# Performance work log

Measured on AMD Instinct MI355X. Metric: run time of the kernel, lower is better.

Reference implementation:

```python
import jax, jax.numpy as jnp
import numpy as np

BETA = 0.25
CODEBOOK_SIZE = 4096
EMBED_DIM = 32


def setup_inputs() -> dict:
    key = jax.random.key(0)
    k_z, k_t = jax.random.split(key)
    z = jax.random.normal(k_z, (16, EMBED_DIM, 64, 64), dtype=jnp.float32)
    table = jax.random.normal(k_t, (CODEBOOK_SIZE, EMBED_DIM), dtype=jnp.float32)
    return {"z": z, "table": table}


def reference(z, table):
    B, C, H, W = z.shape
    # [B,C,H,W] -> [B,H,W,C] -> [N,C]
    z_flat = jnp.transpose(z, (0, 2, 3, 1)).reshape(-1, C)
    # squared-distance: ||z||^2 + ||e||^2 - 2 z.e^T  -> [N, K]
    distances = (
        jnp.sum(z_flat * z_flat, axis=1, keepdims=True)
        + jnp.sum(table * table, axis=1)
        - 2.0 * jnp.einsum("nc,kc->nk", z_flat, table)
    )
    indices = jnp.argmin(distances, axis=1)          # [N]
    z_q_raw = table[indices]                         # [N, C]

    codebook_loss = jnp.mean((jax.lax.stop_gradient(z_flat) - z_q_raw) ** 2)
    commitment_loss = jnp.mean((z_flat - jax.lax.stop_gradient(z_q_raw)) ** 2)
    total_loss = codebook_loss + BETA * commitment_loss

    # straight-through estimator
    z_q = z_flat + jax.lax.stop_gradient(z_q_raw - z_flat)
    z_q = jnp.transpose(z_q.reshape(B, H, W, C), (0, 3, 1, 2))  # [B,C,H,W]
    per_back_indices = indices.reshape(B, -1)
    return z_q, per_back_indices, total_loss
```

## Files before the change

### kernel.cpp

```cpp
#include <hip/hip_runtime.h>
#include <hip/hip_bf16.h>

#define CDIM 32
#define KCODES 4096
#define NROWS 65536
#define HW 4096
#define KP 8
#define KSLICE (KCODES / KP)
#define TPB 256
#define RPT 2
#define ROWS_PER_BLOCK (TPB * RPT)
#define TILE 64
#define BETA 0.25f

#define LOSS_OFF  0u
#define BIAS_OFF  256u
#define SCORE_OFF (256u + KCODES * 4u)
#define IDX_OFF   (SCORE_OFF + (unsigned)KP * NROWS * 4u)
#define Z2_OFF    (IDX_OFF + (unsigned)KP * NROWS * 4u)

__global__ __launch_bounds__(256) void vq_bias(const float* __restrict__ table,
                                               float* __restrict__ bias) {
    int k = blockIdx.x * 256 + threadIdx.x;
    if (k >= KCODES) return;
    const float4* row = (const float4*)(table + (size_t)k * CDIM);
    float s = 0.f;
#pragma unroll
    for (int i = 0; i < CDIM / 4; ++i) {
        float4 v = row[i];
        s = fmaf(v.x, v.x, s);
        s = fmaf(v.y, v.y, s);
        s = fmaf(v.z, v.z, s);
        s = fmaf(v.w, v.w, s);
    }
    bias[k] = -0.5f * s;
}

__global__ __launch_bounds__(TPB) void vq_main(const float* __restrict__ z,
                                               const float* __restrict__ table,
                                               const float* __restrict__ bias,
                                               float* __restrict__ scores,
                                               int* __restrict__ idxs,
                                               float* __restrict__ z2out) {
    __shared__ float elds[TILE * CDIM];
    __shared__ float blds[TILE];

    const int t = threadIdx.x;
    const int rb = blockIdx.x * ROWS_PER_BLOCK;
    const int kp = blockIdx.y;
    const int k0 = kp * KSLICE;
    const int n0 = rb + t;
    const int n1 = n0 + TPB;
    const int b  = rb >> 12;
    const int hw0 = n0 & (HW - 1);
    const int hw1 = n1 & (HW - 1);
    const float* zb = z + (size_t)b * CDIM * HW;

    float z0[CDIM], z1[CDIM];
#pragma unroll
    for (int c = 0; c < CDIM; ++c) {
        z0[c] = zb[c * HW + hw0];
        z1[c] = zb[c * HW + hw1];
    }

    float best0 = -1e30f, best1 = -1e30f;
    int bi0 = 0, bi1 = 0;

    for (int kt = 0; kt < KSLICE; kt += TILE) {
        __syncthreads();
        const float4* src = (const float4*)(table + (size_t)(k0 + kt) * CDIM);
        float4* dst = (float4*)elds;
        dst[t] = src[t];
        dst[t + TPB] = src[t + TPB];
        if (t < TILE) blds[t] = bias[k0 + kt + t];
        __syncthreads();

#pragma unroll 2
        for (int kk = 0; kk < TILE; ++kk) {
            float a0 = blds[kk];
            float a1 = a0;
            const float* e = elds + kk * CDIM;
#pragma unroll
            for (int c = 0; c < CDIM; ++c) {
                float ev = e[c];
                a0 = fmaf(z0[c], ev, a0);
                a1 = fmaf(z1[c], ev, a1);
            }
            int k = k0 + kt + kk;
            if (a0 > best0) { best0 = a0; bi0 = k; }
            if (a1 > best1) { best1 = a1; bi1 = k; }
        }
    }

    scores[kp * NROWS + n0] = best0;
    scores[kp * NROWS + n1] = best1;
    idxs[kp * NROWS + n0] = bi0;
    idxs[kp * NROWS + n1] = bi1;

    if (kp == 0) {
        float s0 = 0.f, s1 = 0.f;
#pragma unroll
        for (int c = 0; c < CDIM; ++c) {
            s0 = fmaf(z0[c], z0[c], s0);
            s1 = fmaf(z1[c], z1[c], s1);
        }
        z2out[n0] = s0;
        z2out[n1] = s1;
    }
}

__global__ __launch_bounds__(256) void vq_combine(const float* __restrict__ scores,
                                                  const int* __restrict__ idxs,
                                                  const float* __restrict__ z2,
                                                  const float* __restrict__ table,
                                                  float* __restrict__ out_zq,
                                                  float* __restrict__ out_idx,
                                                  float* __restrict__ loss) {
    const int n = blockIdx.x * 256 + threadIdx.x;
    float best = -1e30f;
    int bi = 0;
#pragma unroll
    for (int kp = 0; kp < KP; ++kp) {
        float s = scores[kp * NROWS + n];
        int i = idxs[kp * NROWS + n];
        if (s > best) { best = s; bi = i; }
    }

    out_idx[n] = (float)bi;

    const int b = n >> 12;
    const int hw = n & (HW - 1);
    const float4* trow = (const float4*)(table + (size_t)bi * CDIM);
#pragma unroll
    for (int c4 = 0; c4 < CDIM / 4; ++c4) {
        float4 v = trow[c4];
        float* o = out_zq + ((size_t)(b * CDIM + c4 * 4) * HW + hw);
        o[0]        = v.x;
        o[HW]       = v.y;
        o[2 * HW]   = v.z;
        o[3 * HW]   = v.w;
    }

    float d = fmaxf(z2[n] - 2.0f * best, 0.0f);
#pragma unroll
    for (int off = 32; off; off >>= 1) d += __shfl_down(d, off);
    if ((threadIdx.x & 63) == 0) atomicAdd(loss, d);
}

__global__ void vq_finalize(const float* __restrict__ loss,
                            float* __restrict__ out_loss) {
    out_loss[0] = loss[0] * (1.0f + BETA) / (float)((size_t)NROWS * CDIM);
}

extern "C" void kernel_launch(void* const* d_in, const int* in_sizes, int n_in,
                              void* d_out, int out_size, void* d_ws, size_t ws_size,
                              hipStream_t stream) {
    const float* z     = (const float*)d_in[0];
    const float* table = (const float*)d_in[1];

    char* ws = (char*)d_ws;
    float* loss   = (float*)(ws + LOSS_OFF);
    float* bias   = (float*)(ws + BIAS_OFF);
    float* scores = (float*)(ws + SCORE_OFF);
    int*   idxs   = (int*)(ws + IDX_OFF);
    float* z2     = (float*)(ws + Z2_OFF);

    float* out_zq   = (float*)d_out;
    float* out_idx  = out_zq + (size_t)NROWS * CDIM;
    float* out_loss = out_idx + NROWS;

    hipMemsetAsync(loss, 0, sizeof(float), stream);

    vq_bias<<<KCODES / 256, 256, 0, stream>>>(table, bias);

    dim3 grid(NROWS / ROWS_PER_BLOCK, KP);
    vq_main<<<grid, TPB, 0, stream>>>(z, table, bias, scores, idxs, z2);

    vq_combine<<<NROWS / 256, 256, 0, stream>>>(scores, idxs, z2, table,
                                                out_zq, out_idx, loss);

    vq_finalize<<<1, 1, 0, stream>>>(loss, out_loss);
}
```

Measured before the change: 310.3 us.

## Use 2D register-tiled 4x4 outer-product distance kernel without K-split

Replaces the per-thread row scan (each thread holding two z rows, reading codebook entries from LDS) with a 64x64 tile scheme. Each thread computes a 4x4 block of rows by codes as outer products from transposed LDS tiles of z and the codebook. It then does a shuffle-based argmax across the 16 code-lanes with lowest-index tie-breaking. The K-split over 8 slices and its partial-score merge are removed, and the combine kernel now recomputes ||z||^2 from z itself. This raises FMA-to-LDS-load ratio but iterates all 4096 codes per block with a barrier per 64-code tile.

After: 324.0 us. 1.04x slower.

```diff
diff --git a/kernel.cpp b/kernel.cpp
--- a/kernel.cpp
+++ b/kernel.cpp
@@ -5,19 +5,15 @@
 #define KCODES 4096
 #define NROWS 65536
 #define HW 4096
-#define KP 8
-#define KSLICE (KCODES / KP)
 #define TPB 256
-#define RPT 2
-#define ROWS_PER_BLOCK (TPB * RPT)
-#define TILE 64
+#define RTILE 64
+#define KTILE 64
 #define BETA 0.25f
 
 #define LOSS_OFF  0u
 #define BIAS_OFF  256u
-#define SCORE_OFF (256u + KCODES * 4u)
-#define IDX_OFF   (SCORE_OFF + (unsigned)KP * NROWS * 4u)
-#define Z2_OFF    (IDX_OFF + (unsigned)KP * NROWS * 4u)
+#define SCORE_OFF (BIAS_OFF + KCODES * 4u)
+#define IDX_OFF   (SCORE_OFF + (unsigned)NROWS * 4u)
 
 __global__ __launch_bounds__(256) void vq_bias(const float* __restrict__ table,
                                                float* __restrict__ bias) {
@@ -36,112 +32,145 @@
     bias[k] = -0.5f * s;
 }
 
-__global__ __launch_bounds__(TPB) void vq_main(const float* __restrict__ z,
-                                               const float* __restrict__ table,
-                                               const float* __restrict__ bias,
-                                               float* __restrict__ scores,
-                                               int* __restrict__ idxs,
-                                               float* __restrict__ z2out) {
-    __shared__ float elds[TILE * CDIM];
-    __shared__ float blds[TILE];
-
-    const int t = threadIdx.x;
-    const int rb = blockIdx.x * ROWS_PER_BLOCK;
-    const int kp = blockIdx.y;
-    const int k0 = kp * KSLICE;
-    const int n0 = rb + t;
-    const int n1 = n0 + TPB;
-    const int b  = rb >> 12;
-    const int hw0 = n0 & (HW - 1);
-    const int hw1 = n1 & (HW - 1);
-    const float* zb = z + (size_t)b * CDIM * HW;
-
-    float z0[CDIM], z1[CDIM];
-#pragma unroll
-    for (int c = 0; c < CDIM; ++c) {
-        z0[c] = zb[c * HW + hw0];
-        z1[c] = zb[c * HW + hw1];
-    }
-
-    float best0 = -1e30f, best1 = -1e30f;
-    int bi0 = 0, bi1 = 0;
-
-    for (int kt = 0; kt < KSLICE; kt += TILE) {
+__global__ __launch_bounds__(TPB, 4) void vq_main(const float* __restrict__ z,
+                                                  const float* __restrict__ table,
+                                                  const float* __restrict__ bias,
+                                                  float* __restrict__ scores,
+                                                  int* __restrict__ idxs) {
+    __shared__ __align__(16) float zt[CDIM][RTILE];
+    __shared__ __align__(16) float et[CDIM][KTILE];
+    __shared__ __align__(16) float blds[KTILE];
+
+    const int t  = threadIdx.x;
+    const int tx = t & 15;
+    const int ty = t >> 4;
+    const int row0 = blockIdx.x * RTILE;
+    const int b   = row0 >> 12;
+    const int hw0 = row0 & (HW - 1);
+    const float* zb = z + (size_t)b * CDIM * HW + hw0;
+
+    {
+        int c = t >> 4, q = t & 15;
+        float4 v0 = *(const float4*)(zb + (size_t)c * HW + q * 4);
+        *(float4*)&zt[c][q * 4] = v0;
+        float4 v1 = *(const float4*)(zb + (size_t)(c + 16) * HW + q * 4);
+        *(float4*)&zt[c + 16][q * 4] = v1;
+    }
+
+    float best[4] = {-1e30f, -1e30f, -1e30f, -1e30f};
+    int   bi[4]   = {0, 0, 0, 0};
+
+    for (int k0 = 0; k0 < KCODES; k0 += KTILE) {
         __syncthreads();
-        const float4* src = (const float4*)(table + (size_t)(k0 + kt) * CDIM);
-        float4* dst = (float4*)elds;
-        dst[t] = src[t];
-        dst[t + TPB] = src[t + TPB];
-        if (t < TILE) blds[t] = bias[k0 + kt + t];
+        {
+            int k = t & 63, c4 = t >> 6;
+            const float* er = table + (size_t)(k0 + k) * CDIM;
+            float4 v = *(const float4*)(er + c4 * 4);
+            et[c4 * 4 + 0][k] = v.x;
+            et[c4 * 4 + 1][k] = v.y;
+            et[c4 * 4 + 2][k] = v.z;
+            et[c4 * 4 + 3][k] = v.w;
+            float4 w = *(const float4*)(er + (c4 + 4) * 4);
+            et[(c4 + 4) * 4 + 0][k] = w.x;
+            et[(c4 + 4) * 4 + 1][k] = w.y;
+            et[(c4 + 4) * 4 + 2][k] = w.z;
+            et[(c4 + 4) * 4 + 3][k] = w.w;
+            if (t < 16) *(float4*)&blds[t * 4] = *(const float4*)(bias + k0 + t * 4);
+        }
         __syncthreads();
 
-#pragma unroll 2
-        for (int kk = 0; kk < TILE; ++kk) {
-            float a0 = blds[kk];
-            float a1 = a0;
-            const float* e = elds + kk * CDIM;
-#pragma unroll
-            for (int c = 0; c < CDIM; ++c) {
-                float ev = e[c];
-                a0 = fmaf(z0[c], ev, a0);
-                a1 = fmaf(z1[c], ev, a1);
+        float4 bv = *(const float4*)&blds[tx * 4];
+        float acc[4][4];
+#pragma unroll
+        for (int j = 0; j < 4; ++j) {
+            acc[j][0] = bv.x; acc[j][1] = bv.y; acc[j][2] = bv.z; acc[j][3] = bv.w;
+        }
+
+#pragma unroll
+        for (int c = 0; c < CDIM; ++c) {
+            float4 zv = *(const float4*)&zt[c][ty * 4];
+            float4 ev = *(const float4*)&et[c][tx * 4];
+            acc[0][0] = fmaf(zv.x, ev.x, acc[0][0]);
+            acc[0][1] = fmaf(zv.x, ev.y, acc[0][1]);
+            acc[0][2] = fmaf(zv.x, ev.z, acc[0][2]);
+            acc[0][3] = fmaf(zv.x, ev.w, acc[0][3]);
+            acc[1][0] = fmaf(zv.y, ev.x, acc[1][0]);
+            acc[1][1] = fmaf(zv.y, ev.y, acc[1][1]);
+            acc[1][2] = fmaf(zv.y, ev.z, acc[1][2]);
+            acc[1][3] = fmaf(zv.y, ev.w, acc[1][3]);
+            acc[2][0] = fmaf(zv.z, ev.x, acc[2][0]);
+            acc[2][1] = fmaf(zv.z, ev.y, acc[2][1]);
+            acc[2][2] = fmaf(zv.z, ev.z, acc[2][2]);
+            acc[2][3] = fmaf(zv.z, ev.w, acc[2][3]);
+            acc[3][0] = fmaf(zv.w, ev.x, acc[3][0]);
+            acc[3][1] = fmaf(zv.w, ev.y, acc[3][1]);
+            acc[3][2] = fmaf(zv.w, ev.z, acc[3][2]);
+            acc[3][3] = fmaf(zv.w, ev.w, acc[3][3]);
+        }
+
+#pragma unroll
+        for (int j = 0; j < 4; ++j) {
+#pragma unroll
+            for (int i = 0; i < 4; ++i) {
+                int k = k0 + tx * 4 + i;
+                if (acc[j][i] > best[j]) { best[j] = acc[j][i]; bi[j] = k; }
             }
-            int k = k0 + kt + kk;
-            if (a0 > best0) { best0 = a0; bi0 = k; }
-            if (a1 > best1) { best1 = a1; bi1 = k; }
-        }
-    }
-
-    scores[kp * NROWS + n0] = best0;
-    scores[kp * NROWS + n1] = best1;
-    idxs[kp * NROWS + n0] = bi0;
-    idxs[kp * NROWS + n1] = bi1;
-
-    if (kp == 0) {
-        float s0 = 0.f, s1 = 0.f;
-#pragma unroll
-        for (int c = 0; c < CDIM; ++c) {
-            s0 = fmaf(z0[c], z0[c], s0);
-            s1 = fmaf(z1[c], z1[c], s1);
-        }
-        z2out[n0] = s0;
-        z2out[n1] = s1;
+        }
+    }
+
+#pragma unroll
+    for (int j = 0; j < 4; ++j) {
+        float s = best[j];
+        int   i = bi[j];
+#pragma unroll
+        for (int m = 1; m <= 8; m <<= 1) {
+            float s2 = __shfl_xor(s, m);
+            int   i2 = __shfl_xor(i, m);
+            if (s2 > s || (s2 == s && i2 < i)) { s = s2; i = i2; }
+        }
+        if (tx == 0) {
+            int n = row0 + ty * 4 + j;
+            scores[n] = s;
+            idxs[n]   = i;
+        }
     }
 }
 
 __global__ __launch_bounds__(256) void vq_combine(const float* __restrict__ scores,
                                                   const int* __restrict__ idxs,
-                                                  const float* __restrict__ z2,
+                                                  const float* __restrict__ z,
                                                   const float* __restrict__ table,
                                                   float* __restrict__ out_zq,
                                                   float* __restrict__ out_idx,
                                                   float* __restrict__ loss) {
     const int n = blockIdx.x * 256 + threadIdx.x;
-    float best = -1e30f;
-    int bi = 0;
-#pragma unroll
-    for (int kp = 0; kp < KP; ++kp) {
-        float s = scores[kp * NROWS + n];
-        int i = idxs[kp * NROWS + n];
-        if (s > best) { best = s; bi = i; }
-    }
-
-    out_idx[n] = (float)bi;
-
+    const int bi = idxs[n];
+    const float best = scores[n];
     const int b = n >> 12;
     const int hw = n & (HW - 1);
+
+    const float* zb = z + (size_t)b * CDIM * HW + hw;
+    float z2 = 0.f;
+#pragma unroll
+    for (int c = 0; c < CDIM; ++c) {
+        float v = zb[(size_t)c * HW];
+        z2 = fmaf(v, v, z2);
+    }
+
+    out_idx[n] = (float)bi;
+
     const float4* trow = (const float4*)(table + (size_t)bi * CDIM);
+    float* o = out_zq + (size_t)b * CDIM * HW + hw;
 #pragma unroll
     for (int c4 = 0; c4 < CDIM / 4; ++c4) {
         float4 v = trow[c4];
-        float* o = out_zq + ((size_t)(b * CDIM + c4 * 4) * HW + hw);
-        o[0]        = v.x;
-        o[HW]       = v.y;
-        o[2 * HW]   = v.z;
-        o[3 * HW]   = v.w;
-    }
-
-    float d = fmaxf(z2[n] - 2.0f * best, 0.0f);
+        o[(size_t)(c4 * 4 + 0) * HW] = v.x;
+        o[(size_t)(c4 * 4 + 1) * HW] = v.y;
+        o[(size_t)(c4 * 4 + 2) * HW] = v.z;
+        o[(size_t)(c4 * 4 + 3) * HW] = v.w;
+    }
+
+    float d = fmaxf(z2 - 2.0f * best, 0.0f);
 #pragma unroll
     for (int off = 32; off; off >>= 1) d += __shfl_down(d, off);
     if ((threadIdx.x & 63) == 0) atomicAdd(loss, d);
@@ -163,7 +192,6 @@
     float* bias   = (float*)(ws + BIAS_OFF);
     float* scores = (float*)(ws + SCORE_OFF);
     int*   idxs   = (int*)(ws + IDX_OFF);
-    float* z2     = (float*)(ws + Z2_OFF);
 
     float* out_zq   = (float*)d_out;
     float* out_idx  = out_zq + (size_t)NROWS * CDIM;
@@ -172,12 +200,8 @@
     hipMemsetAsync(loss, 0, sizeof(float), stream);
 
     vq_bias<<<KCODES / 256, 256, 0, stream>>>(table, bias);
-
-    dim3 grid(NROWS / ROWS_PER_BLOCK, KP);
-    vq_main<<<grid, TPB, 0, stream>>>(z, table, bias, scores, idxs, z2);
-
-    vq_combine<<<NROWS / 256, 256, 0, stream>>>(scores, idxs, z2, table,
+    vq_main<<<NROWS / RTILE, TPB, 0, stream>>>(z, table, bias, scores, idxs);
+    vq_combine<<<NROWS / 256, 256, 0, stream>>>(scores, idxs, z, table,
                                                 out_zq, out_idx, loss);
-
     vq_finalize<<<1, 1, 0, stream>>>(loss, out_loss);
 }
```

## Replace LDS codebook tiling with wave-uniform global loads and move z-norm to combine

Applied to the files above, without the earlier changes.

The main distance kernel no longer stages codebook tiles in shared memory with barriers. Each thread streams codebook rows directly from global memory at a wave-uniform index, so the compiler can use scalar loads and broadcast operands. Rows are paired as adjacent elements and loaded with float2, and the squared norm of z is computed in the combine kernel instead of a workspace buffer. This trades LDS traffic and synchronization for reliance on the scalar/L1 cache, and adds an extra read of z in combine.

Result: faster. 285.4 us (-8.0%).

```diff
diff --git a/kernel.cpp b/kernel.cpp
--- a/kernel.cpp
+++ b/kernel.cpp
@@ -8,16 +8,12 @@
 #define KP 8
 #define KSLICE (KCODES / KP)
 #define TPB 256
-#define RPT 2
-#define ROWS_PER_BLOCK (TPB * RPT)
-#define TILE 64
 #define BETA 0.25f
 
 #define LOSS_OFF  0u
 #define BIAS_OFF  256u
-#define SCORE_OFF (256u + KCODES * 4u)
+#define SCORE_OFF (BIAS_OFF + KCODES * 4u)
 #define IDX_OFF   (SCORE_OFF + (unsigned)KP * NROWS * 4u)
-#define Z2_OFF    (IDX_OFF + (unsigned)KP * NROWS * 4u)
 
 __global__ __launch_bounds__(256) void vq_bias(const float* __restrict__ table,
                                                float* __restrict__ bias) {
@@ -36,82 +32,54 @@
     bias[k] = -0.5f * s;
 }
 
-__global__ __launch_bounds__(TPB) void vq_main(const float* __restrict__ z,
-                                               const float* __restrict__ table,
-                                               const float* __restrict__ bias,
-                                               float* __restrict__ scores,
-                                               int* __restrict__ idxs,
-                                               float* __restrict__ z2out) {
-    __shared__ float elds[TILE * CDIM];
-    __shared__ float blds[TILE];
-
-    const int t = threadIdx.x;
-    const int rb = blockIdx.x * ROWS_PER_BLOCK;
-    const int kp = blockIdx.y;
-    const int k0 = kp * KSLICE;
-    const int n0 = rb + t;
-    const int n1 = n0 + TPB;
-    const int b  = rb >> 12;
-    const int hw0 = n0 & (HW - 1);
-    const int hw1 = n1 & (HW - 1);
-    const float* zb = z + (size_t)b * CDIM * HW;
+__global__ __launch_bounds__(TPB, 2) void vq_main(const float* __restrict__ z,
+                                                  const float* __restrict__ table,
+                                                  const float* __restrict__ bias,
+                                                  float* __restrict__ scores,
+                                                  int* __restrict__ idxs) {
+    const int t    = threadIdx.x;
+    const int kp   = blockIdx.y;
+    const int row0 = blockIdx.x * (TPB * 2);
+    const int n0   = row0 + t * 2;
+    const int b    = n0 >> 12;
+    const int hw   = n0 & (HW - 1);
+    const float* zb = z + (size_t)b * CDIM * HW + hw;
 
     float z0[CDIM], z1[CDIM];
 #pragma unroll
     for (int c = 0; c < CDIM; ++c) {
-        z0[c] = zb[c * HW + hw0];
-        z1[c] = zb[c * HW + hw1];
+        float2 v = *(const float2*)(zb + (size_t)c * HW);
+        z0[c] = v.x;
+        z1[c] = v.y;
     }
 
     float best0 = -1e30f, best1 = -1e30f;
     int bi0 = 0, bi1 = 0;
 
-    for (int kt = 0; kt < KSLICE; kt += TILE) {
-        __syncthreads();
-        const float4* src = (const float4*)(table + (size_t)(k0 + kt) * CDIM);
-        float4* dst = (float4*)elds;
-        dst[t] = src[t];
-        dst[t + TPB] = src[t + TPB];
-        if (t < TILE) blds[t] = bias[k0 + kt + t];
-        __syncthreads();
-
+    const int kbeg = kp * KSLICE;
+    const int kend = kbeg + KSLICE;
 #pragma unroll 2
-        for (int kk = 0; kk < TILE; ++kk) {
-            float a0 = blds[kk];
-            float a1 = a0;
-            const float* e = elds + kk * CDIM;
+    for (int k = kbeg; k < kend; ++k) {
+        const float* er = table + (size_t)k * CDIM;
+        float a0 = bias[k];
+        float a1 = a0;
 #pragma unroll
-            for (int c = 0; c < CDIM; ++c) {
-                float ev = e[c];
-                a0 = fmaf(z0[c], ev, a0);
-                a1 = fmaf(z1[c], ev, a1);
-            }
-            int k = k0 + kt + kk;
-            if (a0 > best0) { best0 = a0; bi0 = k; }
-            if (a1 > best1) { best1 = a1; bi1 = k; }
+        for (int c = 0; c < CDIM; ++c) {
+            float e = er[c];
+            a0 = fmaf(z0[c], e, a0);
+            a1 = fmaf(z1[c], e, a1);
         }
+        if (a0 > best0) { best0 = a0; bi0 = k; }
+        if (a1 > best1) { best1 = a1; bi1 = k; }
     }
 
-    scores[kp * NROWS + n0] = best0;
-    scores[kp * NROWS + n1] = best1;
-    idxs[kp * NROWS + n0] = bi0;
-    idxs[kp * NROWS + n1] = bi1;
-
-    if (kp == 0) {
-        float s0 = 0.f, s1 = 0.f;
-#pragma unroll
-        for (int c = 0; c < CDIM; ++c) {
-            s0 = fmaf(z0[c], z0[c], s0);
-            s1 = fmaf(z1[c], z1[c], s1);
-        }
-        z2out[n0] = s0;
-        z2out[n1] = s1;
-    }
+    *(float2*)(scores + (size_t)kp * NROWS + n0) = make_float2(best0, best1);
+    *(int2*)(idxs + (size_t)kp * NROWS + n0)     = make_int2(bi0, bi1);
 }
 
 __global__ __launch_bounds__(256) void vq_combine(const float* __restrict__ scores,
                                                   const int* __restrict__ idxs,
-                                                  const float* __restrict__ z2,
+                                                  const float* __restrict__ z,
                                                   const float* __restrict__ table,
                                                   float* __restrict__ out_zq,
                                                   float* __restrict__ out_idx,
@@ -121,27 +89,36 @@
     int bi = 0;
 #pragma unroll
     for (int kp = 0; kp < KP; ++kp) {
-        float s = scores[kp * NROWS + n];
-        int i = idxs[kp * NROWS + n];
+        float s = scores[(size_t)kp * NROWS + n];
+        int   i = idxs[(size_t)kp * NROWS + n];
         if (s > best) { best = s; bi = i; }
+    }
+
+    const int b  = n >> 12;
+    const int hw = n & (HW - 1);
+
+    const float* zbp = z + (size_t)b * CDIM * HW + hw;
+    float z2 = 0.f;
+#pragma unroll
+    for (int c = 0; c < CDIM; ++c) {
+        float v = zbp[(size_t)c * HW];
+        z2 = fmaf(v, v, z2);
     }
 
     out_idx[n] = (float)bi;
 
-    const int b = n >> 12;
-    const int hw = n & (HW - 1);
     const float4* trow = (const float4*)(table + (size_t)bi * CDIM);
+    float* o = out_zq + (size_t)b * CDIM * HW + hw;
 #pragma unroll
     for (int c4 = 0; c4 < CDIM / 4; ++c4) {
         float4 v = trow[c4];
-        float* o = out_zq + ((size_t)(b * CDIM + c4 * 4) * HW + hw);
-        o[0]        = v.x;
-        o[HW]       = v.y;
-        o[2 * HW]   = v.z;
-        o[3 * HW]   = v.w;
+        o[(size_t)(c4 * 4 + 0) * HW] = v.x;
+        o[(size_t)(c4 * 4 + 1) * HW] = v.y;
+        o[(size_t)(c4 * 4 + 2) * HW] = v.z;
+        o[(size_t)(c4 * 4 + 3) * HW] = v.w;
     }
 
-    float d = fmaxf(z2[n] - 2.0f * best, 0.0f);
+    float d = fmaxf(z2 - 2.0f * best, 0.0f);
 #pragma unroll
     for (int off = 32; off; off >>= 1) d += __shfl_down(d, off);
     if ((threadIdx.x & 63) == 0) atomicAdd(loss, d);
@@ -163,7 +140,6 @@
     float* bias   = (float*)(ws + BIAS_OFF);
     float* scores = (float*)(ws + SCORE_OFF);
     int*   idxs   = (int*)(ws + IDX_OFF);
-    float* z2     = (float*)(ws + Z2_OFF);
 
     float* out_zq   = (float*)d_out;
     float* out_idx  = out_zq + (size_t)NROWS * CDIM;
@@ -173,11 +149,10 @@
 
     vq_bias<<<KCODES / 256, 256, 0, stream>>>(table, bias);
 
-    dim3 grid(NROWS / ROWS_PER_BLOCK, KP);
-    vq_main<<<grid, TPB, 0, stream>>>(z, table, bias, scores, idxs, z2);
+    dim3 grid(NROWS / (TPB * 2), KP);
+    vq_main<<<grid, TPB, 0, stream>>>(z, table, bias, scores, idxs);
 
-    vq_combine<<<NROWS / 256, 256, 0, stream>>>(scores, idxs, z2, table,
+    vq_combine<<<NROWS / 256, 256, 0, stream>>>(scores, idxs, z, table,
                                                 out_zq, out_idx, loss);
-
     vq_finalize<<<1, 1, 0, stream>>>(loss, out_loss);
 }
```
